# Optimization experiments

Hardware: AMD Instinct MI355X
Metric: run time of the kernel (lower is better)

## Reference

```python
import jax, jax.numpy as jnp
from jax import lax
import numpy as np

BIN_THR = 0.5
ENDPOINT_THR = 8.0
K_WEIGHT = 60.0
THIN_ITERS = 8  # fixed-iteration Zhang-Suen thinning (stand-in for skimage.skeletonize)


def _bce_with_logits(x, y):
    # elementwise binary_cross_entropy_with_logits, reduction='none'
    return jnp.maximum(x, 0.0) - x * y + jnp.log1p(jnp.exp(-jnp.abs(x)))


def _center_zero_kernel(size):
    k = np.ones((1, 1, size, size), dtype=np.float32)
    k[0, 0, size // 2, size // 2] = 0.0
    return jnp.asarray(k)


def _conv2d(img, kernel, pad):
    # img: [N, 1, H, W], kernel: [1, 1, k, k]
    return lax.conv_general_dilated(img, kernel, (1, 1), [(pad, pad), (pad, pad)])


def _thin_substep(img, sub):
    # img: [N, H, W] of {0,1} float32; one Zhang-Suen sub-iteration (sub is a static int)
    N, H, W = img.shape
    p = jnp.pad(img, ((0, 0), (1, 1), (1, 1)))
    sh = lambda dy, dx: p[:, 1 + dy:1 + dy + H, 1 + dx:1 + dx + W]
    # clockwise neighbors p2..p9: N, NE, E, SE, S, SW, W, NW
    nb = [sh(-1, 0), sh(-1, 1), sh(0, 1), sh(1, 1), sh(1, 0), sh(1, -1), sh(0, -1), sh(-1, -1)]
    Bn = sum(nb)  # neighbor count
    trans = sum(((nb[i] < 0.5) & (nb[(i + 1) % 8] > 0.5)).astype(jnp.int32) for i in range(8))
    c1 = (Bn >= 2.0) & (Bn <= 6.0) & (trans == 1)
    p2, p4, p6, p8 = nb[0], nb[2], nb[4], nb[6]
    if sub == 0:
        c2 = (p2 * p4 * p6 == 0.0) & (p4 * p6 * p8 == 0.0)
    else:
        c2 = (p2 * p4 * p8 == 0.0) & (p2 * p6 * p8 == 0.0)
    delete = (img > 0.5) & c1 & c2
    return jnp.where(delete, 0.0, img)


def _skeletonize(img):
    # img: [N, H, W] binary float32
    def body(i, a):
        a = _thin_substep(a, 0)
        a = _thin_substep(a, 1)
        return a
    return lax.fori_loop(0, THIN_ITERS, body, img)


def setup_inputs() -> dict:
    key = jax.random.key(0)
    kx, ky = jax.random.split(key)
    x = jax.random.normal(kx, (16, 4, 512, 512), dtype=jnp.float32)
    y = jax.random.uniform(ky, (16, 4, 512, 512), dtype=jnp.float32)
    return {"x": x, "y": y}


def reference(x, y):
    Bsz, Np, H, W = x.shape
    loss_map = _bce_with_logits(x, y)  # [B, Np, H, W]
    # binarize: softmax over dim 0, threshold -> {0,1}; detached in original
    s = jax.nn.softmax(x, axis=0)
    A = lax.stop_gradient(jnp.where(s >= BIN_THR, 1.0, 0.0))
    # skeletonize each 2D slice
    skel = _skeletonize(A.reshape(Bsz * Np, H, W))  # [B*Np, H, W]
    # endpoint map: 3x3 ones-with-zero-center conv, threshold at 8
    ep_k = _center_zero_kernel(3)
    c_map = _conv2d(skel[:, None], ep_k, pad=1)  # [B*Np, 1, H, W]
    C = (c_map >= ENDPOINT_THR).astype(jnp.float32)
    # weight map: 9x9 ones-with-zero-center conv * K
    nb_k = _center_zero_kernel(9)
    Wmap = _conv2d(C.reshape(Bsz * Np, 1, H, W), nb_k, pad=4) * K_WEIGHT
    Wmap = Wmap.reshape(Bsz, Np, H, W)
    return jnp.mean(loss_map * Wmap)
```

## Files before the change

kernel.cpp:

```cpp
#include <hip/hip_runtime.h>
#include <cstdint>

#define HH 512
#define WW 512
#define NBATCH 16
#define NPRED 4
#define WPR 8
#define NELEM (NBATCH*NPRED*HH*WW)
#define HALO 21
#define OUTR 64
#define NRTOT (OUTR + 2*HALO)
#define LP (WPR+2)
#define NBLK 512
#define NTHR 256


static __device__ __forceinline__ void fadd(uint64_t a, uint64_t b, uint64_t ci,
                                            uint64_t& s, uint64_t& co) {
    uint64_t x = a ^ b;
    s  = x ^ ci;
    co = (a & b) | (ci & x);
}

static __device__ __forceinline__ void faddio(uint64_t& a, uint64_t b, uint64_t& c) {
    uint64_t x = a ^ b;
    uint64_t s = x ^ c;
    c = (a & b) | (c & x);
    a = s;
}

static __device__ __forceinline__ void sum8(const uint64_t q[8],
                                            uint64_t& b0, uint64_t& b1,
                                            uint64_t& b2, uint64_t& b3) {
    uint64_t s0,c0,s1,c1,s2,c2;
    fadd(q[0],q[1],q[2], s0,c0);
    fadd(q[3],q[4],q[5], s1,c1);
    s2 = q[6] ^ q[7]; c2 = q[6] & q[7];
    uint64_t ca; fadd(s0,s1,s2, b0, ca);
    uint64_t t, cb; fadd(c0,c1,c2, t, cb);
    b1 = t ^ ca; uint64_t cc = t & ca;
    b2 = cb ^ cc; b3 = cb & cc;
}

static __device__ __forceinline__ void acc74(uint64_t w[7], uint64_t b0, uint64_t b1,
                                             uint64_t b2, uint64_t b3) {
    uint64_t c;
    { uint64_t x = w[0] ^ b0; c = w[0] & b0; w[0] = x; }
    faddio(w[1], b1, c);
    faddio(w[2], b2, c);
    faddio(w[3], b3, c);
    { uint64_t x = w[4] ^ c; c = w[4] & c; w[4] = x; }
    { uint64_t x = w[5] ^ c; c = w[5] & c; w[5] = x; }
    w[6] ^= c;
}


__global__ void k_binarize(const float* __restrict__ x, uint64_t* __restrict__ pack) {
    int tid = blockIdx.x * blockDim.x + threadIdx.x;
    int w = tid & (WW-1);
    int h = (tid >> 9) & (HH-1);
    int p = tid >> 18;
    int lane = threadIdx.x & 63;
    float v[NBATCH], e[NBATCH];
    float m = -3.4e38f;
    int base = (p*HH + h)*WW + w;
    #pragma unroll
    for (int b = 0; b < NBATCH; ++b) {
        v[b] = x[(size_t)b*(NPRED*HH*WW) + base];
        m = fmaxf(m, v[b]);
    }
    float S = 0.f;
    #pragma unroll
    for (int b = 0; b < NBATCH; ++b) { e[b] = expf(v[b] - m); S += e[b]; }
    float hS = 0.5f * S;
    unsigned long long mymask = 0ULL;
    #pragma unroll
    for (int b = 0; b < NBATCH; ++b) {
        unsigned long long mk = __ballot(e[b] >= hS);
        if (lane == b) mymask = mk;
    }
    if (lane < NBATCH) {
        int slice = lane * NPRED + p;
        pack[((size_t)slice*HH + h)*WPR + (w >> 6)] = mymask;
    }
}

__global__ __launch_bounds__(NTHR) void k_thin_wmap(const uint64_t* __restrict__ pack,
                                                    const float* __restrict__ x,
                                                    const float* __restrict__ y,
                                                    double* __restrict__ partials) {
    __shared__ uint64_t A[(NRTOT+2)*LP];
    __shared__ uint64_t B[(NRTOT+2)*LP];
    __shared__ uint64_t Hs[4*72*WPR];
    __shared__ int chg[16];
    __shared__ int cflag;
    __shared__ double sdata[NTHR];

    const int s    = blockIdx.x >> 3;
    const int base = (blockIdx.x & 7) << 6;
    const int R0   = base - HALO;
    const int tid  = threadIdx.x;

    for (int i = tid; i < (NRTOT+2)*LP; i += NTHR) { A[i] = 0; B[i] = 0; }
    if (tid < 16) chg[tid] = 0;
    if (tid == 0) cflag = 0;
    __syncthreads();
    for (int i = tid; i < NRTOT*WPR; i += NTHR) {
        int lr = i >> 3, c = i & 7;
        int r = R0 + lr;
        if ((unsigned)r < (unsigned)HH)
            A[(lr+1)*LP + c + 1] = pack[((size_t)s*HH + r)*WPR + c];
    }
    __syncthreads();

    uint64_t* cur = A; uint64_t* nxt = B;
    int stable = 0;
    for (int step = 0; step < 16; ++step) {
        if (stable >= 2) break;
        bool mych = false;
        for (int i = tid; i < NRTOT*WPR; i += NTHR) {
            int lr = i >> 3, c = i & 7;
            int o = (lr+1)*LP + c + 1;
            uint64_t up = cur[o-LP-1], uc = cur[o-LP], un = cur[o-LP+1];
            uint64_t mp = cur[o-1],    mc = cur[o],    mn = cur[o+1];
            uint64_t dp = cur[o+LP-1], dc = cur[o+LP], dn = cur[o+LP+1];
            uint64_t p2 = uc;
            uint64_t p3 = (uc>>1)|(un<<63);
            uint64_t p4 = (mc>>1)|(mn<<63);
            uint64_t p5 = (dc>>1)|(dn<<63);
            uint64_t p6 = dc;
            uint64_t p7 = (dc<<1)|(dp>>63);
            uint64_t p8 = (mc<<1)|(mp>>63);
            uint64_t p9 = (uc<<1)|(up>>63);
            uint64_t qq[8] = {p2,p3,p4,p5,p6,p7,p8,p9};
            uint64_t n0,n1,n2,n3; sum8(qq,n0,n1,n2,n3);
            uint64_t condB = (n1|n2|n3) & ~(n3 | (n2&n1&n0));
            uint64_t tq[8];
            #pragma unroll
            for (int k = 0; k < 8; ++k) tq[k] = ~qq[k] & qq[(k+1)&7];
            uint64_t t0,t1,t2,t3; sum8(tq,t0,t1,t2,t3);
            uint64_t trans1 = t0 & ~(t1|t2|t3);
            uint64_t cond2 = (step & 1) ? (~(p2&p4&p8) & ~(p2&p6&p8))
                                        : (~(p2&p4&p6) & ~(p4&p6&p8));
            uint64_t nv = mc & ~(condB & trans1 & cond2);
            nxt[o] = nv;
            mych |= (nv != mc);
        }
        if (mych) chg[step] = 1;
        __syncthreads();
        stable = chg[step] ? 0 : stable + 1;
        uint64_t* t = cur; cur = nxt; nxt = t;
    }

    uint64_t* Cb = nxt;
    for (int i = tid; i < 72*WPR; i += NTHR) {
        int lr = (i >> 3) + 17, c = i & 7;
        int o = (lr+1)*LP + c + 1;
        uint64_t up = cur[o-LP-1], uc = cur[o-LP], un = cur[o-LP+1];
        uint64_t mp = cur[o-1],    mc = cur[o],    mn = cur[o+1];
        uint64_t dp = cur[o+LP-1], dc = cur[o+LP], dn = cur[o+LP+1];
        uint64_t p3 = (uc>>1)|(un<<63);
        uint64_t p4 = (mc>>1)|(mn<<63);
        uint64_t p5 = (dc>>1)|(dn<<63);
        uint64_t p7 = (dc<<1)|(dp>>63);
        uint64_t p8 = (mc<<1)|(mp>>63);
        uint64_t p9 = (uc<<1)|(up>>63);
        uint64_t cv = uc & p3 & p4 & p5 & dc & p7 & p8 & p9;
        Cb[o] = cv;
        if (cv) cflag = 1;
    }
    __syncthreads();

    if (!cflag) {
        if (tid == 0) partials[blockIdx.x] = 0.0;
        return;
    }

    for (int i = tid; i < 72*WPR; i += NTHR) {
        int hr = i >> 3, c = i & 7;
        int o = (hr+18)*LP + c + 1;
        uint64_t mp = Cb[o-1], mc = Cb[o], mn = Cb[o+1];
        uint64_t m[8];
        m[0] = (mc>>1)|(mn<<63); m[1] = (mc>>2)|(mn<<62);
        m[2] = (mc>>3)|(mn<<61); m[3] = (mc>>4)|(mn<<60);
        m[4] = (mc<<1)|(mp>>63); m[5] = (mc<<2)|(mp>>62);
        m[6] = (mc<<3)|(mp>>61); m[7] = (mc<<4)|(mp>>60);
        uint64_t b0,b1,b2,b3; sum8(m,b0,b1,b2,b3);
        uint64_t inc = mc;
        uint64_t s0 = b0 ^ inc; inc &= b0;
        uint64_t s1 = b1 ^ inc; inc &= b1;
        uint64_t s2 = b2 ^ inc; inc &= b2;
        uint64_t s3 = b3 ^ inc;
        Hs[0*576 + i] = s0; Hs[1*576 + i] = s1;
        Hs[2*576 + i] = s2; Hs[3*576 + i] = s3;
    }
    __syncthreads();

    double acc = 0.0;
    for (int i = tid; i < OUTR*WPR; i += NTHR) {
        int orr = i >> 3, c = i & 7;
        uint64_t w[7];
        int h0 = orr*WPR + c;
        w[0] = Hs[0*576 + h0]; w[1] = Hs[1*576 + h0];
        w[2] = Hs[2*576 + h0]; w[3] = Hs[3*576 + h0];
        w[4] = 0; w[5] = 0; w[6] = 0;
        #pragma unroll
        for (int d = 1; d < 9; ++d) {
            int hh = (orr+d)*WPR + c;
            acc74(w, Hs[0*576+hh], Hs[1*576+hh], Hs[2*576+hh], Hs[3*576+hh]);
        }
        uint64_t cb = Cb[(orr+HALO+1)*LP + c + 1];
        #pragma unroll
        for (int j = 0; j < 7; ++j) {
            uint64_t t = w[j];
            w[j] = t ^ cb;
            cb &= ~t;
        }
        uint64_t any = w[0]|w[1]|w[2]|w[3]|w[4]|w[5]|w[6];
        if (any) {
            size_t pix0 = ((size_t)s*HH + (base + orr))*WW + ((size_t)c << 6);
            uint64_t rem = any;
            while (rem) {
                int bit = __builtin_ctzll(rem);
                rem &= rem - 1;
                int wv = 0;
                #pragma unroll
                for (int j = 0; j < 7; ++j) wv |= (int)((w[j] >> bit) & 1ULL) << j;
                size_t idx = pix0 + bit;
                float lx = x[idx], ly = y[idx];
                float loss = fmaxf(lx, 0.f) - lx*ly + log1pf(expf(-fabsf(lx)));
                acc += (double)(loss * (60.0f * (float)wv));
            }
        }
    }
    sdata[tid] = acc;
    __syncthreads();
    for (int s2 = NTHR/2; s2 > 0; s2 >>= 1) {
        if (tid < s2) sdata[tid] += sdata[tid + s2];
        __syncthreads();
    }
    if (tid == 0) partials[blockIdx.x] = sdata[0];
}

__global__ void k_reduce(const double* __restrict__ partials, float* __restrict__ out,
                         int nparts) {
    __shared__ double sdata[256];
    double a = 0.0;
    for (int i = threadIdx.x; i < nparts; i += 256) a += partials[i];
    sdata[threadIdx.x] = a;
    __syncthreads();
    for (int s2 = 128; s2 > 0; s2 >>= 1) {
        if (threadIdx.x < s2) sdata[threadIdx.x] += sdata[threadIdx.x + s2];
        __syncthreads();
    }
    if (threadIdx.x == 0) out[0] = (float)(sdata[0] / (double)NELEM);
}


extern "C" void kernel_launch(void* const* d_in, const int* in_sizes, int n_in,
                              void* d_out, int out_size, void* d_ws, size_t ws_size,
                              hipStream_t stream) {
    const float* x = (const float*)d_in[0];
    const float* y = (const float*)d_in[1];
    char* ws = (char*)d_ws;
    uint64_t* packA    = (uint64_t*)(ws);
    double*   partials = (double*)  (ws + (2u<<20));

    k_binarize<<<4096, 256, 0, stream>>>(x, packA);
    k_thin_wmap<<<NBLK, NTHR, 0, stream>>>(packA, x, y, partials);
    k_reduce<<<1, 256, 0, stream>>>(partials, (float*)d_out, NBLK);
}
```

Measured before the change: 31.65 us.

## Vectorize binarize kernel with float4 loads and shared-memory nibble transpose

The binarize kernel now has each thread load float4 vectors, so it processes four pixels per batch element. The softmax threshold becomes a log-sum-exp comparison that uses fast intrinsics, which removes the per-element division and the exp storage. Per-thread 4-bit masks are transposed into 64-bit packed words through shared memory, replacing the per-batch wave ballots. The workspace layout is reordered and the grid shrinks 4x. The fast __expf/__logf comparison could flip bits for pixels near the threshold.

```diff
diff --git a/kernel.cpp b/kernel.cpp
--- a/kernel.cpp
+++ b/kernel.cpp
@@ -55,34 +55,47 @@
 }
 
 
-__global__ void k_binarize(const float* __restrict__ x, uint64_t* __restrict__ pack) {
-    int tid = blockIdx.x * blockDim.x + threadIdx.x;
-    int w = tid & (WW-1);
-    int h = (tid >> 9) & (HH-1);
-    int p = tid >> 18;
-    int lane = threadIdx.x & 63;
-    float v[NBATCH], e[NBATCH];
-    float m = -3.4e38f;
-    int base = (p*HH + h)*WW + w;
+__global__ __launch_bounds__(256) void k_binarize(const float* __restrict__ x,
+                                                  uint64_t* __restrict__ pack) {
+    __shared__ uint64_t nibs[272];
+    const int t = blockIdx.x * 256 + threadIdx.x;
+    const float4* __restrict__ xv = reinterpret_cast<const float4*>(x);
+    float4 va[NBATCH];
+    #pragma unroll
+    for (int b = 0; b < NBATCH; ++b) va[b] = xv[(size_t)b * (NPRED*HH*WW/4) + t];
+    float4 mx = va[0];
+    #pragma unroll
+    for (int b = 1; b < NBATCH; ++b) {
+        mx.x = fmaxf(mx.x, va[b].x); mx.y = fmaxf(mx.y, va[b].y);
+        mx.z = fmaxf(mx.z, va[b].z); mx.w = fmaxf(mx.w, va[b].w);
+    }
+    float sx=0.f, sy=0.f, sz=0.f, sw=0.f;
     #pragma unroll
     for (int b = 0; b < NBATCH; ++b) {
-        v[b] = x[(size_t)b*(NPRED*HH*WW) + base];
-        m = fmaxf(m, v[b]);
-    }
-    float S = 0.f;
-    #pragma unroll
-    for (int b = 0; b < NBATCH; ++b) { e[b] = expf(v[b] - m); S += e[b]; }
-    float hS = 0.5f * S;
-    unsigned long long mymask = 0ULL;
+        sx += __expf(va[b].x - mx.x); sy += __expf(va[b].y - mx.y);
+        sz += __expf(va[b].z - mx.z); sw += __expf(va[b].w - mx.w);
+    }
+    const float tx = mx.x + __logf(0.5f*sx), ty = mx.y + __logf(0.5f*sy);
+    const float tz = mx.z + __logf(0.5f*sz), tw = mx.w + __logf(0.5f*sw);
+    uint64_t nib = 0;
     #pragma unroll
     for (int b = 0; b < NBATCH; ++b) {
-        unsigned long long mk = __ballot(e[b] >= hS);
-        if (lane == b) mymask = mk;
-    }
-    if (lane < NBATCH) {
-        int slice = lane * NPRED + p;
-        pack[((size_t)slice*HH + h)*WPR + (w >> 6)] = mymask;
-    }
+        unsigned n = (va[b].x >= tx ? 1u:0u) | (va[b].y >= ty ? 2u:0u)
+                   | (va[b].z >= tz ? 4u:0u) | (va[b].w >= tw ? 8u:0u);
+        nib |= (uint64_t)n << (4*b);
+    }
+    nibs[threadIdx.x + (threadIdx.x >> 4)] = nib;
+    __syncthreads();
+    const int wg = threadIdx.x >> 4, b = threadIdx.x & 15;
+    uint64_t word = 0;
+    #pragma unroll
+    for (int j = 0; j < 16; ++j)
+        word |= ((nibs[wg*17 + j] >> (4*b)) & 0xFULL) << (4*j);
+    const int wgg = blockIdx.x * 16 + wg;
+    const int wword = wgg & 7;
+    const int h = (wgg >> 3) & (HH-1);
+    const int p = wgg >> 12;
+    pack[((size_t)(b*NPRED + p)*HH + h)*WPR + wword] = word;
 }
 
 __global__ __launch_bounds__(NTHR) void k_thin_wmap(const uint64_t* __restrict__ pack,
@@ -263,10 +276,10 @@
     const float* x = (const float*)d_in[0];
     const float* y = (const float*)d_in[1];
     char* ws = (char*)d_ws;
-    uint64_t* packA    = (uint64_t*)(ws);
-    double*   partials = (double*)  (ws + (2u<<20));
-
-    k_binarize<<<4096, 256, 0, stream>>>(x, packA);
+    double*   partials = (double*)(ws);
+    uint64_t* packA    = (uint64_t*)(ws + 16384);
+
+    k_binarize<<<1024, 256, 0, stream>>>(x, packA);
     k_thin_wmap<<<NBLK, NTHR, 0, stream>>>(packA, x, y, partials);
     k_reduce<<<1, 256, 0, stream>>>(partials, (float*)d_out, NBLK);
 }
```

Result: no change. 31.15 us (-1.6%).
